# Performance work log

Hardware: AMD Instinct MI355X
Metric: run time of the kernel (lower is better)

The kernel has to match this reference:

```python
import jax, jax.numpy as jnp
import numpy as np

N = 50000      # nodes
E = 800000     # edges
IN = 128       # in_dim
H = 128        # hidden_dim
OUT = 64       # out_dim
B = 6          # block_num
NEG_SLOPE = 0.01  # nn.LeakyReLU default


def setup_inputs() -> dict:
    key = jax.random.key(0)
    ks = jax.random.split(key, 10)
    s = 0.05
    return {
        "inputs": jax.random.normal(ks[0], (N, IN), jnp.float32),
        "edges": jax.random.randint(ks[1], (2, E), 0, N, jnp.int32),
        "w_in": jax.random.normal(ks[2], (IN, H), jnp.float32) * s,
        "b_in": jnp.zeros((H,), jnp.float32),
        "w1": jax.random.normal(ks[3], (B, H, H), jnp.float32) * s,
        "b1": jnp.zeros((B, H), jnp.float32),
        "w2": jax.random.normal(ks[4], (B, H, H), jnp.float32) * s,
        "b2": jnp.zeros((B, H), jnp.float32),
        "w_out": jax.random.normal(ks[5], (H, OUT), jnp.float32) * s,
        "b_out": jnp.zeros((OUT,), jnp.float32),
    }


def _leaky(x):
    return jnp.where(x >= 0, x, NEG_SLOPE * x)


def _gcn_conv(x, W, b, src, dst, norm):
    # GCNConv: out = D^{-1/2}(A+I)D^{-1/2} (x W) + b, with self-loops folded in.
    xw = x @ W                                   # [N, d_out]
    msg = xw[src] * norm[src, None]              # gather + edge scaling [E, d_out]
    agg = jax.ops.segment_sum(msg, dst, num_segments=N)
    agg = agg * norm[:, None] + xw * (norm * norm)[:, None]  # neighbors + self-loop
    return agg + b


def reference(inputs, edges, w_in, b_in, w1, b1, w2, b2, w_out, b_out):
    src, dst = edges[0], edges[1]
    deg = 1.0 + jax.ops.segment_sum(jnp.ones((E,), inputs.dtype), dst, num_segments=N)
    norm = jax.lax.rsqrt(deg)                    # [N]

    x = _leaky(_gcn_conv(inputs, w_in, b_in, src, dst, norm))
    for i in range(B):  # fixed small layer loop (structurally distinct params)
        h = _leaky(_gcn_conv(x, w1[i], b1[i], src, dst, norm))
        h = _leaky(_gcn_conv(h, w2[i], b2[i], src, dst, norm))
        x = (x + h) * 0.5
    # dropout in eval mode -> identity
    x_out = _gcn_conv(x, w_out, b_out, src, dst, norm)
    return (x_out, x)
```

## Files before the change

kernel.cpp:

```cpp
#include <hip/hip_runtime.h>

#define NNODES 50000
#define NPAD   50048
#define NEDGES 800000
#define HDIM 128
#define OUTDIM 64

#define GEMM_GRID 196
#define GEMM_BLK  512
#define GEMM_WAVES (GEMM_GRID * (GEMM_BLK / 64))
#define GEMM_TILES (NPAD / 16)

typedef short short8 __attribute__((ext_vector_type(8)));
typedef _Float16 half8 __attribute__((ext_vector_type(8)));
typedef _Float16 half4 __attribute__((ext_vector_type(4)));
typedef float f32x4 __attribute__((ext_vector_type(4)));

__device__ __forceinline__ unsigned short f2bf(float f) {
    unsigned int u = __builtin_bit_cast(unsigned int, f);
    unsigned int r = (u + 0x7FFFu + ((u >> 16) & 1u)) >> 16;
    return (unsigned short)r;
}
__device__ __forceinline__ float bf2f(unsigned short b) {
    unsigned int u = ((unsigned int)b) << 16;
    return __builtin_bit_cast(float, u);
}

__global__ void count_kernel(const int* __restrict__ dst, int* __restrict__ deg,
                             int* __restrict__ epos) {
    int e = blockIdx.x * 256 + threadIdx.x;
    if (e < NEDGES) epos[e] = atomicAdd(&deg[dst[e]], 1);
}

__global__ __launch_bounds__(256) void bsum_kernel(const int* __restrict__ deg,
                                                   int* __restrict__ bsum) {
    __shared__ int red[256];
    int i = blockIdx.x * 256 + threadIdx.x;
    red[threadIdx.x] = (i < NNODES) ? deg[i] : 0;
    __syncthreads();
    for (int off = 128; off; off >>= 1) {
        if (threadIdx.x < off) red[threadIdx.x] += red[threadIdx.x + off];
        __syncthreads();
    }
    if (threadIdx.x == 0) bsum[blockIdx.x] = red[0];
}

__global__ __launch_bounds__(256) void bscan_kernel(const int* __restrict__ bsum,
                                                    int* __restrict__ bofs) {
    __shared__ int s[256];
    int t = threadIdx.x;
    int v = (t < 196) ? bsum[t] : 0;
    s[t] = v;
    __syncthreads();
    for (int off = 1; off < 256; off <<= 1) {
        int u = (t >= off) ? s[t - off] : 0;
        __syncthreads();
        s[t] += u;
        __syncthreads();
    }
    if (t < 196) bofs[t] = s[t] - v;
}

__global__ __launch_bounds__(256) void emit_kernel(
    const int* __restrict__ deg, const int* __restrict__ bofs,
    int* __restrict__ row_ptr, float* __restrict__ norm) {
    __shared__ int s[256];
    int t = threadIdx.x;
    int i = blockIdx.x * 256 + t;
    int v = (i < NNODES) ? deg[i] : 0;
    s[t] = v;
    __syncthreads();
    for (int off = 1; off < 256; off <<= 1) {
        int u = (t >= off) ? s[t - off] : 0;
        __syncthreads();
        s[t] += u;
        __syncthreads();
    }
    int excl = s[t] - v + bofs[blockIdx.x];
    if (i < NNODES) {
        row_ptr[i] = excl;
        norm[i] = rsqrtf(1.0f + (float)v);
    }
    if (i == NNODES - 1) row_ptr[NNODES] = NEDGES;
}

__global__ void fill_kernel(const int* __restrict__ src, const int* __restrict__ dst,
                            const int* __restrict__ epos, const int* __restrict__ row_ptr,
                            int* __restrict__ sorted_src) {
    int e = blockIdx.x * 256 + threadIdx.x;
    if (e < NEDGES) sorted_src[row_ptr[dst[e]] + epos[e]] = src[e];
}

__global__ __launch_bounds__(256) void prep_w_kernel(
    const float* __restrict__ w_in, const float* __restrict__ w1,
    const float* __restrict__ w2, const float* __restrict__ w_out,
    unsigned short* __restrict__ wT, _Float16* __restrict__ w2f) {
    int idx = blockIdx.x * 256 + threadIdx.x;
    if (idx < 16384 + 98304) {
        const float* W;
        unsigned short* o;
        int e;
        if (idx < 16384) {
            W = w_in; o = wT; e = idx;
        } else {
            int j = idx - 16384; int m = j >> 14; e = j & 16383;
            W = w1 + ((size_t)m << 14); o = wT + (size_t)(1 + m) * 32768;
        }
        int k = e >> 7, n = e & 127;
        float v = W[e];
        unsigned short h = f2bf(v);
        o[(size_t)n * 256 + k] = h;
        o[(size_t)n * 256 + 128 + k] = f2bf(v - bf2f(h));
    } else if (idx < 16384 + 196608) {
        int j = idx - 16384 - 98304; int m = j >> 14; int e = j & 16383;
        int k = e >> 7, n = e & 127;
        w2f[(size_t)m * 16384 + n * 128 + k] = (_Float16)w2[((size_t)m << 14) + e];
    } else {
        int e = idx - 212992;
        int k = e >> 6, n = e & 63;
        float v = w_out[e];
        unsigned short h = f2bf(v);
        unsigned short* o = wT + (size_t)7 * 32768;
        o[(size_t)n * 256 + k] = h;
        o[(size_t)n * 256 + 128 + k] = f2bf(v - bf2f(h));
    }
}

__global__ __launch_bounds__(256) void split_x_kernel(
    const float* __restrict__ x, unsigned short* __restrict__ xc) {
    int gid = blockIdx.x * 256 + threadIdx.x;
    int row = gid >> 6;
    int kk = (gid & 63) * 2;
    float2 v = {0.f, 0.f};
    if (row < NNODES) v = *(const float2*)(x + (size_t)row * 128 + kk);
    unsigned short h0 = f2bf(v.x), h1 = f2bf(v.y);
    unsigned short l0 = f2bf(v.x - bf2f(h0)), l1 = f2bf(v.y - bf2f(h1));
    *(unsigned int*)(xc + (size_t)row * 256 + kk) =
        (unsigned int)h0 | ((unsigned int)h1 << 16);
    *(unsigned int*)(xc + (size_t)row * 256 + 128 + kk) =
        (unsigned int)l0 | ((unsigned int)l1 << 16);
}

template <int NCOLS>
__global__ __launch_bounds__(GEMM_BLK) void gemm_bf_kernel(
    const unsigned short* __restrict__ xc, const unsigned short* __restrict__ wT,
    const float* __restrict__ norm, _Float16* __restrict__ y) {
    __shared__ unsigned short Blds[NCOLS * 256];
    const int t = threadIdx.x;
    const int wave = t >> 6, lane = t & 63, quad = lane >> 4, l16 = lane & 15;

    constexpr int NCH = NCOLS * 32;
#pragma unroll
    for (int i = 0; i < NCH / GEMM_BLK; ++i) {
        int C = i * GEMM_BLK + t;
        int n = C >> 5, c = C & 31;
        const unsigned short* gp = wT + ((size_t)n << 8) + ((c ^ (n & 7)) << 3);
        unsigned short* lp = Blds + ((size_t)C << 3);
        __builtin_amdgcn_global_load_lds(
            (const __attribute__((address_space(1))) void*)gp,
            (__attribute__((address_space(3))) void*)lp, 16, 0, 0);
    }
    __syncthreads();

    const int wid = blockIdx.x * (GEMM_BLK / 64) + wave;
    const int sw = l16 & 7;
    const bool has1 = (wid + GEMM_WAVES) < GEMM_TILES;
    const int rb0 = wid * 16;
    const int rb1 = has1 ? (wid + GEMM_WAVES) * 16 : 0;

    short8 a0[8], a1[8];
    const unsigned short* ap0 = xc + ((size_t)(rb0 + l16) << 8) + quad * 8;
    const unsigned short* ap1 = xc + ((size_t)(rb1 + l16) << 8) + quad * 8;
#pragma unroll
    for (int ck = 0; ck < 8; ++ck) a0[ck] = *(const short8*)(ap0 + ck * 32);
#pragma unroll
    for (int ck = 0; ck < 8; ++ck) a1[ck] = *(const short8*)(ap1 + ck * 32);

    float nm0[4], nm1[4];
#pragma unroll
    for (int r = 0; r < 4; ++r) {
        int r0 = rb0 + quad * 4 + r;
        int r1 = rb1 + quad * 4 + r;
        nm0[r] = norm[r0 < NNODES ? r0 : 0];
        nm1[r] = norm[r1 < NNODES ? r1 : 0];
    }

#pragma unroll
    for (int nt = 0; nt < NCOLS / 16; ++nt) {
        const unsigned short* bp = Blds + ((size_t)(nt * 16 + l16) << 8);
        short8 bh[4], bl[4];
#pragma unroll
        for (int ck = 0; ck < 4; ++ck) {
            bh[ck] = *(const short8*)(bp + (((ck * 4 + quad) ^ sw) << 3));
            bl[ck] = *(const short8*)(bp + (((16 + ck * 4 + quad) ^ sw) << 3));
        }
        f32x4 ac0 = (f32x4){0.f, 0.f, 0.f, 0.f};
        f32x4 ac1 = (f32x4){0.f, 0.f, 0.f, 0.f};
#pragma unroll
        for (int ck = 0; ck < 4; ++ck) {
            ac0 = __builtin_amdgcn_mfma_f32_16x16x32_bf16(a0[ck], bh[ck], ac0, 0, 0, 0);
            ac1 = __builtin_amdgcn_mfma_f32_16x16x32_bf16(a1[ck], bh[ck], ac1, 0, 0, 0);
            ac0 = __builtin_amdgcn_mfma_f32_16x16x32_bf16(a0[ck], bl[ck], ac0, 0, 0, 0);
            ac1 = __builtin_amdgcn_mfma_f32_16x16x32_bf16(a1[ck], bl[ck], ac1, 0, 0, 0);
            ac0 = __builtin_amdgcn_mfma_f32_16x16x32_bf16(a0[4 + ck], bh[ck], ac0, 0, 0, 0);
            ac1 = __builtin_amdgcn_mfma_f32_16x16x32_bf16(a1[4 + ck], bh[ck], ac1, 0, 0, 0);
        }
        int col = nt * 16 + l16;
#pragma unroll
        for (int r = 0; r < 4; ++r) {
            int r0 = rb0 + quad * 4 + r;
            if (r0 < NNODES) y[(size_t)r0 * NCOLS + col] = (_Float16)(ac0[r] * nm0[r]);
            int r1 = rb1 + quad * 4 + r;
            if (has1 && r1 < NNODES) y[(size_t)r1 * NCOLS + col] = (_Float16)(ac1[r] * nm1[r]);
        }
    }
}

__global__ __launch_bounds__(GEMM_BLK) void gemm_f16_kernel(
    const _Float16* __restrict__ A, const _Float16* __restrict__ wf,
    const float* __restrict__ norm, _Float16* __restrict__ y) {
    __shared__ _Float16 Blds[128 * 128];
    const int t = threadIdx.x;
    const int wave = t >> 6, lane = t & 63, quad = lane >> 4, l16 = lane & 15;

#pragma unroll
    for (int i = 0; i < 2048 / GEMM_BLK; ++i) {
        int C = i * GEMM_BLK + t;
        int n = C >> 4, c = C & 15;
        const _Float16* gp = wf + ((size_t)n << 7) + ((c ^ (n & 7)) << 3);
        _Float16* lp = Blds + ((size_t)C << 3);
        __builtin_amdgcn_global_load_lds(
            (const __attribute__((address_space(1))) void*)gp,
            (__attribute__((address_space(3))) void*)lp, 16, 0, 0);
    }
    __syncthreads();

    const int wid = blockIdx.x * (GEMM_BLK / 64) + wave;
    const int sw = l16 & 7;
    const bool has1 = (wid + GEMM_WAVES) < GEMM_TILES;
    const int rb0 = wid * 16;
    const int rb1 = has1 ? (wid + GEMM_WAVES) * 16 : 0;

    half8 a0[4], a1[4];
    const _Float16* ap0 = A + ((size_t)(rb0 + l16) << 7) + quad * 8;
    const _Float16* ap1 = A + ((size_t)(rb1 + l16) << 7) + quad * 8;
#pragma unroll
    for (int ck = 0; ck < 4; ++ck) a0[ck] = *(const half8*)(ap0 + ck * 32);
#pragma unroll
    for (int ck = 0; ck < 4; ++ck) a1[ck] = *(const half8*)(ap1 + ck * 32);

    float nm0[4], nm1[4];
#pragma unroll
    for (int r = 0; r < 4; ++r) {
        int r0 = rb0 + quad * 4 + r;
        int r1 = rb1 + quad * 4 + r;
        nm0[r] = norm[r0 < NNODES ? r0 : 0];
        nm1[r] = norm[r1 < NNODES ? r1 : 0];
    }

#pragma unroll
    for (int nt = 0; nt < 8; ++nt) {
        const _Float16* bp = Blds + ((size_t)(nt * 16 + l16) << 7);
        half8 b[4];
#pragma unroll
        for (int ck = 0; ck < 4; ++ck)
            b[ck] = *(const half8*)(bp + (((ck * 4 + quad) ^ sw) << 3));
        f32x4 ac0 = (f32x4){0.f, 0.f, 0.f, 0.f};
        f32x4 ac1 = (f32x4){0.f, 0.f, 0.f, 0.f};
#pragma unroll
        for (int ck = 0; ck < 4; ++ck) {
            ac0 = __builtin_amdgcn_mfma_f32_16x16x32_f16(a0[ck], b[ck], ac0, 0, 0, 0);
            ac1 = __builtin_amdgcn_mfma_f32_16x16x32_f16(a1[ck], b[ck], ac1, 0, 0, 0);
        }
        int col = nt * 16 + l16;
#pragma unroll
        for (int r = 0; r < 4; ++r) {
            int r0 = rb0 + quad * 4 + r;
            if (r0 < NNODES) y[(size_t)r0 * 128 + col] = (_Float16)(ac0[r] * nm0[r]);
            int r1 = rb1 + quad * 4 + r;
            if (has1 && r1 < NNODES) y[(size_t)r1 * 128 + col] = (_Float16)(ac1[r] * nm1[r]);
        }
    }
}

template <int MODE, bool WOUT, bool OUT16>
__global__ __launch_bounds__(256) void gather_fin128(
    const _Float16* __restrict__ y, const int* __restrict__ row_ptr,
    const int* __restrict__ sorted_src, const float* __restrict__ norm,
    const float* __restrict__ bias, const unsigned short* __restrict__ xcres,
    float* __restrict__ out, unsigned short* __restrict__ xcout,
    _Float16* __restrict__ h16) {
    const int wave = threadIdx.x >> 6;
    const int lane = threadIdx.x & 63;
    const int g = lane >> 4, j = lane & 15;
    const int n = blockIdx.x * 16 + wave * 4 + g;
    const int beg = row_ptr[n];
    const int deg = row_ptr[n + 1] - beg;
    int dmax = deg;
    dmax = max(dmax, __shfl_xor(dmax, 16));
    dmax = max(dmax, __shfl_xor(dmax, 32));

    float acc[8];
#pragma unroll
    for (int c = 0; c < 8; ++c) acc[c] = 0.f;

    for (int i = 0; i < dmax; i += 8) {
        int sarr[8];
#pragma unroll
        for (int u = 0; u < 8; ++u)
            sarr[u] = (i + u < deg) ? sorted_src[beg + i + u] : -1;
        half8 h[8];
#pragma unroll
        for (int u = 0; u < 8; ++u)
            if (sarr[u] >= 0)
                h[u] = *(const half8*)(y + ((size_t)sarr[u] << 7) + j * 8);
#pragma unroll
        for (int u = 0; u < 8; ++u)
            if (sarr[u] >= 0) {
#pragma unroll
                for (int c = 0; c < 8; ++c) acc[c] += (float)h[u][c];
            }
    }

    const half8 sh = *(const half8*)(y + ((size_t)n << 7) + j * 8);
    const float4 b0 = *(const float4*)(bias + j * 8);
    const float4 b1 = *(const float4*)(bias + j * 8 + 4);
    const float bb[8] = {b0.x, b0.y, b0.z, b0.w, b1.x, b1.y, b1.z, b1.w};
    const float nm = norm[n];
    float v[8];
#pragma unroll
    for (int c = 0; c < 8; ++c) {
        float t = (acc[c] + (float)sh[c]) * nm + bb[c];
        v[c] = t >= 0.f ? t : 0.01f * t;
    }
    if (MODE == 1) {
        short8 hw = *(const short8*)(xcres + ((size_t)n << 8) + j * 8);
        short8 lw = *(const short8*)(xcres + ((size_t)n << 8) + 128 + j * 8);
#pragma unroll
        for (int c = 0; c < 8; ++c) {
            float xr = bf2f((unsigned short)hw[c]) + bf2f((unsigned short)lw[c]);
            v[c] = (xr + v[c]) * 0.5f;
        }
    }
    if (WOUT) {
        float4 o0 = {v[0], v[1], v[2], v[3]};
        float4 o1 = {v[4], v[5], v[6], v[7]};
        *(float4*)(out + ((size_t)n << 7) + j * 8) = o0;
        *(float4*)(out + ((size_t)n << 7) + j * 8 + 4) = o1;
    }
    if (OUT16) {
        half8 o;
#pragma unroll
        for (int c = 0; c < 8; ++c) o[c] = (_Float16)v[c];
        *(half8*)(h16 + ((size_t)n << 7) + j * 8) = o;
    } else {
        short8 hi, lo;
#pragma unroll
        for (int c = 0; c < 8; ++c) {
            unsigned short hv = f2bf(v[c]);
            hi[c] = (short)hv;
            lo[c] = (short)f2bf(v[c] - bf2f(hv));
        }
        *(short8*)(xcout + ((size_t)n << 8) + j * 8) = hi;
        *(short8*)(xcout + ((size_t)n << 8) + 128 + j * 8) = lo;
    }
}

__global__ __launch_bounds__(256) void gather_fin64(
    const _Float16* __restrict__ y, const int* __restrict__ row_ptr,
    const int* __restrict__ sorted_src, const float* __restrict__ norm,
    const float* __restrict__ bias, float* __restrict__ out) {
    const int wave = threadIdx.x >> 6;
    const int lane = threadIdx.x & 63;
    const int g = lane >> 4, j = lane & 15;
    const int n = blockIdx.x * 16 + wave * 4 + g;
    const int beg = row_ptr[n];
    const int deg = row_ptr[n + 1] - beg;
    int dmax = deg;
    dmax = max(dmax, __shfl_xor(dmax, 16));
    dmax = max(dmax, __shfl_xor(dmax, 32));

    float acc[4] = {0.f, 0.f, 0.f, 0.f};
    for (int i = 0; i < dmax; i += 8) {
        int sarr[8];
#pragma unroll
        for (int u = 0; u < 8; ++u)
            sarr[u] = (i + u < deg) ? sorted_src[beg + i + u] : -1;
        half4 h[8];
#pragma unroll
        for (int u = 0; u < 8; ++u)
            if (sarr[u] >= 0)
                h[u] = *(const half4*)(y + ((size_t)sarr[u] << 6) + j * 4);
#pragma unroll
        for (int u = 0; u < 8; ++u)
            if (sarr[u] >= 0) {
#pragma unroll
                for (int c = 0; c < 4; ++c) acc[c] += (float)h[u][c];
            }
    }

    const half4 sh = *(const half4*)(y + ((size_t)n << 6) + j * 4);
    const float4 b = *(const float4*)(bias + j * 4);
    const float bb[4] = {b.x, b.y, b.z, b.w};
    const float nm = norm[n];
    float4 o;
    o.x = (acc[0] + (float)sh[0]) * nm + bb[0];
    o.y = (acc[1] + (float)sh[1]) * nm + bb[1];
    o.z = (acc[2] + (float)sh[2]) * nm + bb[2];
    o.w = (acc[3] + (float)sh[3]) * nm + bb[3];
    *(float4*)(out + ((size_t)n << 6) + j * 4) = o;
}

extern "C" void kernel_launch(void* const* d_in, const int* in_sizes, int n_in,
                              void* d_out, int out_size, void* d_ws, size_t ws_size,
                              hipStream_t stream) {
    const float* inputs = (const float*)d_in[0];
    const int* edges = (const int*)d_in[1];
    const int* src = edges;
    const int* dst = edges + NEDGES;
    const float* w_in  = (const float*)d_in[2];
    const float* b_in  = (const float*)d_in[3];
    const float* w1    = (const float*)d_in[4];
    const float* b1    = (const float*)d_in[5];
    const float* w2    = (const float*)d_in[6];
    const float* b2    = (const float*)d_in[7];
    const float* w_out = (const float*)d_in[8];
    const float* b_out = (const float*)d_in[9];

    float* out  = (float*)d_out;
    float* xout = out;
    float* x    = out + (size_t)NNODES * OUTDIM;

    char* p = (char*)d_ws;
    auto alloc = [&](size_t bytes) {
        char* r = p;
        p += (bytes + 63) & ~(size_t)63;
        return r;
    };
    int* deg        = (int*)alloc(NNODES * 4);
    int* epos       = (int*)alloc(NEDGES * 4);
    int* row_ptr    = (int*)alloc((NNODES + 1) * 4);
    int* bsum       = (int*)alloc(256 * 4);
    int* bofs       = (int*)alloc(256 * 4);
    int* sorted_src = (int*)alloc(NEDGES * 4);
    float* normb    = (float*)alloc(NNODES * 4);
    unsigned short* wT = (unsigned short*)alloc((size_t)245760 * 2);
    _Float16* w2f   = (_Float16*)alloc((size_t)6 * 16384 * 2);
    unsigned short* xc_x = (unsigned short*)alloc((size_t)NPAD * 256 * 2);
    unsigned short* xc_in = (unsigned short*)alloc((size_t)NPAD * 256 * 2);
    _Float16* h16   = (_Float16*)alloc((size_t)NPAD * 128 * 2);
    _Float16* y     = (_Float16*)alloc((size_t)NNODES * HDIM * 2);

    hipMemsetAsync(deg, 0, NNODES * sizeof(int), stream);
    count_kernel<<<(NEDGES + 255) / 256, 256, 0, stream>>>(dst, deg, epos);
    bsum_kernel<<<196, 256, 0, stream>>>(deg, bsum);
    bscan_kernel<<<1, 256, 0, stream>>>(bsum, bofs);
    emit_kernel<<<196, 256, 0, stream>>>(deg, bofs, row_ptr, normb);
    fill_kernel<<<(NEDGES + 255) / 256, 256, 0, stream>>>(src, dst, epos, row_ptr, sorted_src);
    prep_w_kernel<<<864, 256, 0, stream>>>(w_in, w1, w2, w_out, wT, w2f);

    split_x_kernel<<<(NPAD * 64) / 256, 256, 0, stream>>>(inputs, xc_in);
    gemm_bf_kernel<128><<<GEMM_GRID, GEMM_BLK, 0, stream>>>(xc_in, wT, normb, y);
    gather_fin128<0, false, false><<<NNODES / 16, 256, 0, stream>>>(
        y, row_ptr, sorted_src, normb, b_in, nullptr, nullptr, xc_x, nullptr);

    for (int i = 0; i < 6; ++i) {
        gemm_bf_kernel<128><<<GEMM_GRID, GEMM_BLK, 0, stream>>>(
            xc_x, wT + (size_t)(1 + i) * 32768, normb, y);
        gather_fin128<0, false, true><<<NNODES / 16, 256, 0, stream>>>(
            y, row_ptr, sorted_src, normb, b1 + i * HDIM, nullptr, nullptr, nullptr, h16);
        gemm_f16_kernel<<<GEMM_GRID, GEMM_BLK, 0, stream>>>(
            h16, w2f + (size_t)i * 16384, normb, y);
        if (i < 5)
            gather_fin128<1, false, false><<<NNODES / 16, 256, 0, stream>>>(
                y, row_ptr, sorted_src, normb, b2 + i * HDIM, xc_x, nullptr, xc_x, nullptr);
        else
            gather_fin128<1, true, false><<<NNODES / 16, 256, 0, stream>>>(
                y, row_ptr, sorted_src, normb, b2 + i * HDIM, xc_x, x, xc_x, nullptr);
    }

    gemm_bf_kernel<64><<<GEMM_GRID, GEMM_BLK, 0, stream>>>(
        xc_x, wT + (size_t)7 * 32768, normb, y);
    gather_fin64<<<NNODES / 16, 256, 0, stream>>>(
        y, row_ptr, sorted_src, normb, b_out, xout);
}
```

Baseline: 788.1 us.

## Use one row tile per GEMM wave, vectorize gather accumulation, add nontemporal accesses

The GEMM kernels now give each wave a single 16-row tile and double the grid to 391 blocks (391*8 waves covers all 3128 tiles). This replaces the previous two-tiles-per-wave scheme, lowering register pressure and spreading the work over more waves. The gather kernels switch to vector float accumulators via convertvector, and the residual reads and fp32 output writes become nontemporal loads and stores to reduce cache pollution. In exchange, each block's LDS weight load now serves half as many rows, so weight staging traffic doubles.

After: 784.4 us. No clear change (-0.5%).

```diff
diff --git a/kernel.cpp b/kernel.cpp
--- a/kernel.cpp
+++ b/kernel.cpp
@@ -6,15 +6,15 @@
 #define HDIM 128
 #define OUTDIM 64
 
-#define GEMM_GRID 196
+#define GEMM_GRID 391
 #define GEMM_BLK  512
-#define GEMM_WAVES (GEMM_GRID * (GEMM_BLK / 64))
 #define GEMM_TILES (NPAD / 16)
 
 typedef short short8 __attribute__((ext_vector_type(8)));
 typedef _Float16 half8 __attribute__((ext_vector_type(8)));
 typedef _Float16 half4 __attribute__((ext_vector_type(4)));
 typedef float f32x4 __attribute__((ext_vector_type(4)));
+typedef float f32x8 __attribute__((ext_vector_type(8)));
 
 __device__ __forceinline__ unsigned short f2bf(float f) {
     unsigned int u = __builtin_bit_cast(unsigned int, f);
@@ -164,25 +164,18 @@
 
     const int wid = blockIdx.x * (GEMM_BLK / 64) + wave;
     const int sw = l16 & 7;
-    const bool has1 = (wid + GEMM_WAVES) < GEMM_TILES;
     const int rb0 = wid * 16;
-    const int rb1 = has1 ? (wid + GEMM_WAVES) * 16 : 0;
-
-    short8 a0[8], a1[8];
+
+    short8 a0[8];
     const unsigned short* ap0 = xc + ((size_t)(rb0 + l16) << 8) + quad * 8;
-    const unsigned short* ap1 = xc + ((size_t)(rb1 + l16) << 8) + quad * 8;
 #pragma unroll
     for (int ck = 0; ck < 8; ++ck) a0[ck] = *(const short8*)(ap0 + ck * 32);
-#pragma unroll
-    for (int ck = 0; ck < 8; ++ck) a1[ck] = *(const short8*)(ap1 + ck * 32);
-
-    float nm0[4], nm1[4];
+
+    float nm0[4];
 #pragma unroll
     for (int r = 0; r < 4; ++r) {
         int r0 = rb0 + quad * 4 + r;
-        int r1 = rb1 + quad * 4 + r;
         nm0[r] = norm[r0 < NNODES ? r0 : 0];
-        nm1[r] = norm[r1 < NNODES ? r1 : 0];
     }
 
 #pragma unroll
@@ -195,23 +188,17 @@
             bl[ck] = *(const short8*)(bp + (((16 + ck * 4 + quad) ^ sw) << 3));
         }
         f32x4 ac0 = (f32x4){0.f, 0.f, 0.f, 0.f};
-        f32x4 ac1 = (f32x4){0.f, 0.f, 0.f, 0.f};
 #pragma unroll
         for (int ck = 0; ck < 4; ++ck) {
             ac0 = __builtin_amdgcn_mfma_f32_16x16x32_bf16(a0[ck], bh[ck], ac0, 0, 0, 0);
-            ac1 = __builtin_amdgcn_mfma_f32_16x16x32_bf16(a1[ck], bh[ck], ac1, 0, 0, 0);
             ac0 = __builtin_amdgcn_mfma_f32_16x16x32_bf16(a0[ck], bl[ck], ac0, 0, 0, 0);
-            ac1 = __builtin_amdgcn_mfma_f32_16x16x32_bf16(a1[ck], bl[ck], ac1, 0, 0, 0);
             ac0 = __builtin_amdgcn_mfma_f32_16x16x32_bf16(a0[4 + ck], bh[ck], ac0, 0, 0, 0);
-            ac1 = __builtin_amdgcn_mfma_f32_16x16x32_bf16(a1[4 + ck], bh[ck], ac1, 0, 0, 0);
         }
         int col = nt * 16 + l16;
 #pragma unroll
         for (int r = 0; r < 4; ++r) {
             int r0 = rb0 + quad * 4 + r;
             if (r0 < NNODES) y[(size_t)r0 * NCOLS + col] = (_Float16)(ac0[r] * nm0[r]);
-            int r1 = rb1 + quad * 4 + r;
-            if (has1 && r1 < NNODES) y[(size_t)r1 * NCOLS + col] = (_Float16)(ac1[r] * nm1[r]);
         }
     }
 }
@@ -237,25 +224,18 @@
 
     const int wid = blockIdx.x * (GEMM_BLK / 64) + wave;
     const int sw = l16 & 7;
-    const bool has1 = (wid + GEMM_WAVES) < GEMM_TILES;
     const int rb0 = wid * 16;
-    const int rb1 = has1 ? (wid + GEMM_WAVES) * 16 : 0;
-
-    half8 a0[4], a1[4];
+
+    half8 a0[4];
     const _Float16* ap0 = A + ((size_t)(rb0 + l16) << 7) + quad * 8;
-    const _Float16* ap1 = A + ((size_t)(rb1 + l16) << 7) + quad * 8;
 #pragma unroll
     for (int ck = 0; ck < 4; ++ck) a0[ck] = *(const half8*)(ap0 + ck * 32);
-#pragma unroll
-    for (int ck = 0; ck < 4; ++ck) a1[ck] = *(const half8*)(ap1 + ck * 32);
-
-    float nm0[4], nm1[4];
+
+    float nm0[4];
 #pragma unroll
     for (int r = 0; r < 4; ++r) {
         int r0 = rb0 + quad * 4 + r;
-        int r1 = rb1 + quad * 4 + r;
         nm0[r] = norm[r0 < NNODES ? r0 : 0];
-        nm1[r] = norm[r1 < NNODES ? r1 : 0];
     }
 
 #pragma unroll
@@ -266,19 +246,14 @@
         for (int ck = 0; ck < 4; ++ck)
             b[ck] = *(const half8*)(bp + (((ck * 4 + quad) ^ sw) << 3));
         f32x4 ac0 = (f32x4){0.f, 0.f, 0.f, 0.f};
-        f32x4 ac1 = (f32x4){0.f, 0.f, 0.f, 0.f};
-#pragma unroll
-        for (int ck = 0; ck < 4; ++ck) {
+#pragma unroll
+        for (int ck = 0; ck < 4; ++ck)
             ac0 = __builtin_amdgcn_mfma_f32_16x16x32_f16(a0[ck], b[ck], ac0, 0, 0, 0);
-            ac1 = __builtin_amdgcn_mfma_f32_16x16x32_f16(a1[ck], b[ck], ac1, 0, 0, 0);
-        }
         int col = nt * 16 + l16;
 #pragma unroll
         for (int r = 0; r < 4; ++r) {
             int r0 = rb0 + quad * 4 + r;
             if (r0 < NNODES) y[(size_t)r0 * 128 + col] = (_Float16)(ac0[r] * nm0[r]);
-            int r1 = rb1 + quad * 4 + r;
-            if (has1 && r1 < NNODES) y[(size_t)r1 * 128 + col] = (_Float16)(ac1[r] * nm1[r]);
         }
     }
 }
@@ -300,9 +275,7 @@
     dmax = max(dmax, __shfl_xor(dmax, 16));
     dmax = max(dmax, __shfl_xor(dmax, 32));
 
-    float acc[8];
-#pragma unroll
-    for (int c = 0; c < 8; ++c) acc[c] = 0.f;
+    f32x8 acc = (f32x8){0.f, 0.f, 0.f, 0.f, 0.f, 0.f, 0.f, 0.f};
 
     for (int i = 0; i < dmax; i += 8) {
         int sarr[8];
@@ -316,16 +289,13 @@
                 h[u] = *(const half8*)(y + ((size_t)sarr[u] << 7) + j * 8);
 #pragma unroll
         for (int u = 0; u < 8; ++u)
-            if (sarr[u] >= 0) {
-#pragma unroll
-                for (int c = 0; c < 8; ++c) acc[c] += (float)h[u][c];
-            }
+            if (sarr[u] >= 0) acc += __builtin_convertvector(h[u], f32x8);
     }
 
     const half8 sh = *(const half8*)(y + ((size_t)n << 7) + j * 8);
-    const float4 b0 = *(const float4*)(bias + j * 8);
-    const float4 b1 = *(const float4*)(bias + j * 8 + 4);
-    const float bb[8] = {b0.x, b0.y, b0.z, b0.w, b1.x, b1.y, b1.z, b1.w};
+    const f32x4 b0 = *(const f32x4*)(bias + j * 8);
+    const f32x4 b1 = *(const f32x4*)(bias + j * 8 + 4);
+    const float bb[8] = {b0[0], b0[1], b0[2], b0[3], b1[0], b1[1], b1[2], b1[3]};
     const float nm = norm[n];
     float v[8];
 #pragma unroll
@@ -334,8 +304,10 @@
         v[c] = t >= 0.f ? t : 0.01f * t;
     }
     if (MODE == 1) {
-        short8 hw = *(const short8*)(xcres + ((size_t)n << 8) + j * 8);
-        short8 lw = *(const short8*)(xcres + ((size_t)n << 8) + 128 + j * 8);
+        short8 hw = __builtin_nontemporal_load(
+            (const short8*)(xcres + ((size_t)n << 8) + j * 8));
+        short8 lw = __builtin_nontemporal_load(
+            (const short8*)(xcres + ((size_t)n << 8) + 128 + j * 8));
 #pragma unroll
         for (int c = 0; c < 8; ++c) {
             float xr = bf2f((unsigned short)hw[c]) + bf2f((unsigned short)lw[c]);
@@ -343,10 +315,10 @@
         }
     }
     if (WOUT) {
-        float4 o0 = {v[0], v[1], v[2], v[3]};
-        float4 o1 = {v[4], v[5], v[6], v[7]};
-        *(float4*)(out + ((size_t)n << 7) + j * 8) = o0;
-        *(float4*)(out + ((size_t)n << 7) + j * 8 + 4) = o1;
+        f32x4 o0 = (f32x4){v[0], v[1], v[2], v[3]};
+        f32x4 o1 = (f32x4){v[4], v[5], v[6], v[7]};
+        __builtin_nontemporal_store(o0, (f32x4*)(out + ((size_t)n << 7) + j * 8));
+        __builtin_nontemporal_store(o1, (f32x4*)(out + ((size_t)n << 7) + j * 8 + 4));
     }
     if (OUT16) {
         half8 o;
@@ -380,7 +352,7 @@
     dmax = max(dmax, __shfl_xor(dmax, 16));
     dmax = max(dmax, __shfl_xor(dmax, 32));
 
-    float acc[4] = {0.f, 0.f, 0.f, 0.f};
+    f32x4 acc = (f32x4){0.f, 0.f, 0.f, 0.f};
     for (int i = 0; i < dmax; i += 8) {
         int sarr[8];
 #pragma unroll
@@ -393,22 +365,18 @@
                 h[u] = *(const half4*)(y + ((size_t)sarr[u] << 6) + j * 4);
 #pragma unroll
         for (int u = 0; u < 8; ++u)
-            if (sarr[u] >= 0) {
-#pragma unroll
-                for (int c = 0; c < 4; ++c) acc[c] += (float)h[u][c];
-            }
+            if (sarr[u] >= 0) acc += __builtin_convertvector(h[u], f32x4);
     }
 
     const half4 sh = *(const half4*)(y + ((size_t)n << 6) + j * 4);
-    const float4 b = *(const float4*)(bias + j * 4);
-    const float bb[4] = {b.x, b.y, b.z, b.w};
+    const f32x4 b = *(const f32x4*)(bias + j * 4);
     const float nm = norm[n];
-    float4 o;
-    o.x = (acc[0] + (float)sh[0]) * nm + bb[0];
-    o.y = (acc[1] + (float)sh[1]) * nm + bb[1];
-    o.z = (acc[2] + (float)sh[2]) * nm + bb[2];
-    o.w = (acc[3] + (float)sh[3]) * nm + bb[3];
-    *(float4*)(out + ((size_t)n << 6) + j * 4) = o;
+    f32x4 o;
+    o[0] = (acc[0] + (float)sh[0]) * nm + b[0];
+    o[1] = (acc[1] + (float)sh[1]) * nm + b[1];
+    o[2] = (acc[2] + (float)sh[2]) * nm + b[2];
+    o[3] = (acc[3] + (float)sh[3]) * nm + b[3];
+    __builtin_nontemporal_store(o, (f32x4*)(out + ((size_t)n << 6) + j * 4));
 }
 
 extern "C" void kernel_launch(void* const* d_in, const int* in_sizes, int n_in,
```
